# Kernel optimization log

Measured on AMD Instinct MI355X. Metric: run time of the kernel, lower is better.

The kernel has to match this reference:

```python
import jax, jax.numpy as jnp
import numpy as np

EPS = 1e-6

def ln(x):
    m = jnp.mean(x, axis=-1, keepdims=True)
    v = jnp.var(x, axis=-1, keepdims=True)
    return (x - m) * jax.lax.rsqrt(v + EPS)

def modulate(x, shift, scale):
    return x * (1.0 + scale[:, None, :]) + shift[:, None, :]

def setup_inputs() -> dict:
    key = jax.random.key(0)
    ks = jax.random.split(key, 16)
    B, N, H = 2, 384, 256
    D = 128  # n_vector_features * scale_dist_features
    MIN = 2 * H + D  # 640
    FH = 1024  # swiglu_correction_fn(4.0, 256)
    s = 0.02
    inp = {
        "mask": jnp.ones((B, N), jnp.float32),
        "x": jax.random.normal(ks[0], (B, N, H), jnp.float32),
        "t_emb": jax.random.normal(ks[1], (B, H), jnp.float32),
        "dist": jax.random.normal(ks[2], (B, N, N, D), jnp.float32),
        "edge_mask": jnp.ones((B, N, N), jnp.float32),
        "W_ada": jax.random.normal(ks[3], (6 * H, H), jnp.float32) * s,
        "b_ada": jnp.zeros((6 * H,), jnp.float32),
        "W_fe1": jax.random.normal(ks[4], (H, MIN), jnp.float32) * s,
        "b_fe1": jnp.zeros((H,), jnp.float32),
        "W_fe2": jax.random.normal(ks[5], (H, H), jnp.float32) * s,
        "b_fe2": jnp.zeros((H,), jnp.float32),
        "W_qkv": jax.random.normal(ks[6], (3 * H, H), jnp.float32) * s,
        "W_out": jax.random.normal(ks[7], (H, H), jnp.float32) * s,
        "W_ffn1": jax.random.normal(ks[8], (2 * FH, H), jnp.float32) * s,
        "W_ffn2": jax.random.normal(ks[9], (H, FH), jnp.float32) * s,
    }
    return inp

def reference(mask, x, t_emb, dist, edge_mask, W_ada, b_ada, W_fe1, b_fe1,
              W_fe2, b_fe2, W_qkv, W_out, W_ffn1, W_ffn2):
    B, N, H = x.shape
    num_heads = 8
    d_head = H // num_heads
    mN = mask[..., None]  # (B,N,1)

    # adaLN modulation
    ada = jax.nn.silu(t_emb) @ W_ada.T + b_ada  # (B,6H)
    shift_msa, scale_msa, gate_msa, shift_mlp, scale_mlp, gate_mlp = jnp.split(ada, 6, axis=1)

    x_norm = modulate(ln(x * mN), shift_msa, scale_msa)  # (B,N,H)

    # all-pairs message passing: concat(h_i, h_j, dist_ij) -> MLP -> sum_j
    h1 = jnp.broadcast_to(x_norm[:, :, None, :], (B, N, N, H))
    h2 = jnp.broadcast_to(x_norm[:, None, :, :], (B, N, N, H))
    feats = jnp.concatenate([h1, h2, dist], axis=-1) * edge_mask[..., None]
    msgs = jax.nn.silu(feats @ W_fe1.T + b_fe1) @ W_fe2.T + b_fe2  # (B,N,N,H)
    x_msg = jnp.sum(msgs, axis=-2)  # (B,N,H)

    # attention
    qkv = x_msg @ W_qkv.T
    Q, K, V = jnp.split(qkv, 3, axis=-1)
    Q = ln(Q * mN)
    K = ln(K * mN)
    def heads(t):
        return t.reshape(B, N, num_heads, d_head).transpose(0, 2, 1, 3)  # b h s d
    Q, K, V = heads(Q), heads(K), heads(V)
    scores = jnp.einsum("bhqd,bhkd->bhqk", Q, K) / jnp.sqrt(jnp.float32(d_head))
    bias = jnp.where(mask[:, None, None, :] > 0, 0.0, -1e9)
    attn = jax.nn.softmax(scores + bias, axis=-1)
    ao = jnp.einsum("bhqk,bhkd->bhqd", attn, V)
    ao = ao.transpose(0, 2, 1, 3).reshape(B, N, H)
    y = ao @ W_out.T

    x = x + gate_msa[:, None, :] * y

    # SwiGLU FFN
    xm = modulate(ln(x * mN), shift_mlp, scale_mlp)
    h12 = xm @ W_ffn1.T
    h_a, h_b = jnp.split(h12, 2, axis=-1)
    ffn_out = (jax.nn.silu(h_a) * h_b) @ W_ffn2.T
    x = (x + gate_mlp[:, None, :] * ffn_out) * mN
    return x
```

## Files before the change

### kernel.cpp

```cpp
#include <hip/hip_runtime.h>

#define DEVI __device__ __forceinline__

typedef float fv4 __attribute__((ext_vector_type(4)));
typedef __bf16 bf16x8 __attribute__((ext_vector_type(8)));
typedef unsigned short u16x8 __attribute__((ext_vector_type(8)));
typedef unsigned short u16x4 __attribute__((ext_vector_type(4)));

DEVI fv4 ldv4(const float* p) { return *reinterpret_cast<const fv4*>(p); }
DEVI bf16x8 pkbf(fv4 a, fv4 b) {
  bf16x8 r;
  r[0] = (__bf16)a[0]; r[1] = (__bf16)a[1]; r[2] = (__bf16)a[2]; r[3] = (__bf16)a[3];
  r[4] = (__bf16)b[0]; r[5] = (__bf16)b[1]; r[6] = (__bf16)b[2]; r[7] = (__bf16)b[3];
  return r;
}
DEVI u16x8 b2u(bf16x8 v) { return __builtin_bit_cast(u16x8, v); }
DEVI bf16x8 asbf(u16x8 u) { return __builtin_bit_cast(bf16x8, u); }
DEVI unsigned short bfbits(float x) { __bf16 v = (__bf16)x; return __builtin_bit_cast(unsigned short, v); }
DEVI u16x4 pk4(fv4 a) {
  u16x4 u;
  u[0] = bfbits(a[0]); u[1] = bfbits(a[1]); u[2] = bfbits(a[2]); u[3] = bfbits(a[3]);
  return u;
}
DEVI fv4 MFMA16(bf16x8 a, bf16x8 b, fv4 c) {
  return __builtin_amdgcn_mfma_f32_16x16x32_bf16(a, b, c, 0, 0, 0);
}
DEVI float siluf(float x) {
  float e = __builtin_amdgcn_exp2f(x * -1.44269504f);
  return x * __builtin_amdgcn_rcpf(1.f + e);
}
DEVI fv4 glu4(fv4 x, fv4 y) {
  fv4 r;
#pragma unroll
  for (int j = 0; j < 4; ++j) r[j] = siluf(x[j]) * y[j];
  return r;
}
DEVI void lbar() {
  asm volatile("s_waitcnt lgkmcnt(0)" ::: "memory");
  __builtin_amdgcn_s_barrier();
}
DEVI int swz(int row, int k) {
  int unit = k >> 3;
  int phys = (unit & ~7) | ((unit ^ row) & 7);
  return row * 384 + (phys << 3) + (k & 7);
}

__global__ __launch_bounds__(256)
void k_ada(const float* __restrict__ temb, const float* __restrict__ W_ada,
           const float* __restrict__ b_ada, float* __restrict__ ada) {
  __shared__ float sm[256];
  const int b = blockIdx.x / 6;
  const int r = (blockIdx.x % 6) * 256 + threadIdx.x;
  sm[threadIdx.x] = siluf(temb[b * 256 + threadIdx.x]);
  __syncthreads();
  float s = b_ada[r];
  const float* wr = W_ada + (size_t)r * 256;
  for (int k = 0; k < 256; ++k) s += sm[k] * wr[k];
  ada[b * 1536 + r] = s;
}

__global__ __launch_bounds__(256)
void k_xnorm(const float* __restrict__ xin, const float* __restrict__ mask,
             const float* __restrict__ ada, int shift_off, int scale_off,
             float* __restrict__ out) {
  const int row = blockIdx.x;
  const int b = row / 384;
  const int t = threadIdx.x;
  const float m = mask[row];
  const float v = xin[(size_t)row * 256 + t] * m;
  float s = v, ss = v * v;
#pragma unroll
  for (int o = 1; o < 64; o <<= 1) { s += __shfl_xor(s, o); ss += __shfl_xor(ss, o); }
  __shared__ float red[8];
  const int wid = t >> 6;
  if ((t & 63) == 0) { red[wid] = s; red[4 + wid] = ss; }
  __syncthreads();
  s = red[0] + red[1] + red[2] + red[3];
  ss = red[4] + red[5] + red[6] + red[7];
  const float mean = s * (1.f / 256.f);
  const float var = ss * (1.f / 256.f) - mean * mean;
  const float rs = rsqrtf(var + 1e-6f);
  out[(size_t)row * 256 + t] =
      (v - mean) * rs * (1.f + ada[b * 1536 + scale_off + t]) + ada[b * 1536 + shift_off + t];
}

template <int EPI, int AMODE>
__global__ __launch_bounds__(256)
void k_gemm(const float* __restrict__ A, int lda,
            const float* __restrict__ B, int ldb, int koff, int K,
            float* __restrict__ C, int ldc,
            const float* __restrict__ bias, float bscale,
            const float* __restrict__ res,
            const float* __restrict__ ada, int gate_off,
            const float* __restrict__ mask) {
  __shared__ __align__(16) unsigned short As[64 * 64];
  __shared__ __align__(16) unsigned short Bs[64 * 64];
  const int t = threadIdx.x, lane = t & 63, w = t >> 6;
  const int bn0 = blockIdx.x * 64, bm0 = blockIdx.y * 64;
  const int qr = (w >> 1) * 32, qc = (w & 1) * 32;
  const int g = lane >> 4, c = lane & 15;
  const int srow = t >> 2;
  const int so = (t & 3) * 2;
  const int o0 = so ^ (srow & 7), o1 = (so + 1) ^ (srow & 7);
  unsigned short* aw0 = As + srow * 64 + o0 * 8;
  unsigned short* aw1 = As + srow * 64 + o1 * 8;
  unsigned short* bw0 = Bs + srow * 64 + o0 * 8;
  unsigned short* bw1 = Bs + srow * 64 + o1 * 8;
  const float* ag = A + (size_t)(bm0 + srow) * lda + so * 8;
  const float* bg = B + (size_t)(bn0 + srow) * ldb + koff + so * 8;
  const float* a2g = nullptr;
  if constexpr (AMODE == 2) a2g = res + ((size_t)(bm0 + srow) * lda + so * 8);
  fv4 a0 = ldv4(ag), a1 = ldv4(ag + 4), a2 = ldv4(ag + 8), a3 = ldv4(ag + 12);
  fv4 x0, x1, x2, x3;
  if constexpr (AMODE == 1) {
    x0 = ldv4(ag + 1024); x1 = ldv4(ag + 1028); x2 = ldv4(ag + 1032); x3 = ldv4(ag + 1036);
  }
  if constexpr (AMODE == 2) {
    x0 = ldv4(a2g); x1 = ldv4(a2g + 4); x2 = ldv4(a2g + 8); x3 = ldv4(a2g + 12);
  }
  fv4 c0 = ldv4(bg), c1 = ldv4(bg + 4), c2 = ldv4(bg + 8), c3 = ldv4(bg + 12);
  fv4 acc[2][2] = {};
  for (int k0 = 0; k0 < K; k0 += 64) {
    lbar();
    if constexpr (AMODE == 1) {
      *reinterpret_cast<u16x8*>(aw0) = b2u(pkbf(glu4(a0, x0), glu4(a1, x1)));
      *reinterpret_cast<u16x8*>(aw1) = b2u(pkbf(glu4(a2, x2), glu4(a3, x3)));
    } else if constexpr (AMODE == 2) {
      *reinterpret_cast<u16x8*>(aw0) = b2u(pkbf(a0 + x0, a1 + x1));
      *reinterpret_cast<u16x8*>(aw1) = b2u(pkbf(a2 + x2, a3 + x3));
    } else {
      *reinterpret_cast<u16x8*>(aw0) = b2u(pkbf(a0, a1));
      *reinterpret_cast<u16x8*>(aw1) = b2u(pkbf(a2, a3));
    }
    *reinterpret_cast<u16x8*>(bw0) = b2u(pkbf(c0, c1));
    *reinterpret_cast<u16x8*>(bw1) = b2u(pkbf(c2, c3));
    lbar();
    if (k0 + 64 < K) {
      ag += 64; bg += 64;
      a0 = ldv4(ag); a1 = ldv4(ag + 4); a2 = ldv4(ag + 8); a3 = ldv4(ag + 12);
      if constexpr (AMODE == 1) {
        x0 = ldv4(ag + 1024); x1 = ldv4(ag + 1028); x2 = ldv4(ag + 1032); x3 = ldv4(ag + 1036);
      }
      if constexpr (AMODE == 2) {
        a2g += 64;
        x0 = ldv4(a2g); x1 = ldv4(a2g + 4); x2 = ldv4(a2g + 8); x3 = ldv4(a2g + 12);
      }
      c0 = ldv4(bg); c1 = ldv4(bg + 4); c2 = ldv4(bg + 8); c3 = ldv4(bg + 12);
    }
#pragma unroll
    for (int kk = 0; kk < 2; ++kk) {
      bf16x8 af[2], bf[2];
#pragma unroll
      for (int mi = 0; mi < 2; ++mi) {
        int row = qr + mi * 16 + c;
        int oct = (kk * 4 + g) ^ (row & 7);
        af[mi] = asbf(*reinterpret_cast<const u16x8*>(As + row * 64 + oct * 8));
      }
#pragma unroll
      for (int ni = 0; ni < 2; ++ni) {
        int row = qc + ni * 16 + c;
        int oct = (kk * 4 + g) ^ (row & 7);
        bf[ni] = asbf(*reinterpret_cast<const u16x8*>(Bs + row * 64 + oct * 8));
      }
#pragma unroll
      for (int mi = 0; mi < 2; ++mi)
#pragma unroll
        for (int ni = 0; ni < 2; ++ni)
          acc[mi][ni] = MFMA16(af[mi], bf[ni], acc[mi][ni]);
    }
  }
#pragma unroll
  for (int mi = 0; mi < 2; ++mi)
#pragma unroll
    for (int ni = 0; ni < 2; ++ni)
#pragma unroll
      for (int r = 0; r < 4; ++r) {
        int row = bm0 + qr + mi * 16 + g * 4 + r;
        int col = bn0 + qc + ni * 16 + c;
        float v = acc[mi][ni][r];
        if constexpr (EPI == 1) v += bscale * bias[col];
        if constexpr (EPI == 2) v = res[(size_t)row * 256 + col] + ada[(row / 384) * 1536 + gate_off + col] * v;
        if constexpr (EPI == 3) v = (res[(size_t)row * 256 + col] + ada[(row / 384) * 1536 + gate_off + col] * v) * mask[row];
        if constexpr (EPI == 5) C[(((size_t)(row >> 4) * 256 + col) << 4) + (row & 15)] = v;
        else C[(size_t)row * ldc + col] = v;
      }
}

__global__ __launch_bounds__(512)
void k_edge(const float* __restrict__ dist, const float* __restrict__ emask,
            const float* __restrict__ Wfe1, const float* __restrict__ bfe1,
            const float* __restrict__ P, const float* __restrict__ Qc,
            float* __restrict__ S0, float* __restrict__ S1) {
  const int blk = blockIdx.x, jh = blockIdx.y;
  const int b = blk / 384, i = blk - b * 384;
  const int t = threadIdx.x, lane = t & 63, w = t >> 6;
  const int g = lane >> 4, c = lane & 15;
  __shared__ __align__(16) unsigned short Al[2][16 * 128];

  bf16x8 Bf[2][4];
  float Pl[2], bl[2], Ss[2] = {0.f, 0.f};
#pragma unroll
  for (int ht = 0; ht < 2; ++ht) {
    const int h = w * 32 + ht * 16 + c;
    const float* wp = Wfe1 + (size_t)h * 640 + 512 + g * 8;
#pragma unroll
    for (int ks = 0; ks < 4; ++ks)
      Bf[ht][ks] = pkbf(ldv4(wp + ks * 32), ldv4(wp + ks * 32 + 4));
    Pl[ht] = P[(size_t)(b * 384 + i) * 256 + h];
    bl[ht] = bfe1[h];
  }
  const float* dbase = dist + (size_t)(b * 384 + i) * 49152 + (size_t)jh * 24576;
  const float* embase = emask + (size_t)(b * 384 + i) * 384 + jh * 192;
  const int jcb = b * 24 + jh * 12;
  const int h0 = w * 32 + c, h1 = h0 + 16;

  const int srow = t >> 5, kq = t & 31;
  const int sunit = kq >> 1;
  const int sphys = (sunit & 8) | ((sunit ^ (srow & 7)) & 7);
  const int soff = srow * 128 + sphys * 8 + (kq & 1) * 4;

  fv4 rX, rY, qvX0, qvX1, qvY0, qvY1, emX, emY;
  {
    fv4 t0 = ldv4(dbase + t * 4);
    *reinterpret_cast<u16x4*>(&Al[0][soff]) = pk4(t0);
  }
  rX = ldv4(dbase + 2048 + t * 4);
  qvX0 = ldv4(Qc + (((size_t)jcb * 256 + h0) << 4) + g * 4);
  qvX1 = ldv4(Qc + (((size_t)jcb * 256 + h1) << 4) + g * 4);
  emX = ldv4(embase + g * 4);
  lbar();

#pragma unroll 1
  for (int p = 0; p < 6; ++p) {
    {
      const int cl = 2 * p;
      if (cl <= 9) rY = ldv4(dbase + (size_t)(cl + 2) * 2048 + t * 4);
      if (cl <= 10) {
        *reinterpret_cast<u16x4*>(&Al[1][soff]) = pk4(rX);
        const size_t jc = (size_t)(jcb + cl + 1);
        qvY0 = ldv4(Qc + ((jc * 256 + h0) << 4) + g * 4);
        qvY1 = ldv4(Qc + ((jc * 256 + h1) << 4) + g * 4);
        emY = ldv4(embase + (cl + 1) * 16 + g * 4);
      }
      fv4 acc0, acc1;
#pragma unroll
      for (int r = 0; r < 4; ++r) { acc0[r] = Pl[0] + qvX0[r]; acc1[r] = Pl[1] + qvX1[r]; }
#pragma unroll
      for (int ks = 0; ks < 4; ++ks) {
        const int u = ks * 4 + g;
        const int phys = (u & 8) | ((u ^ (c & 7)) & 7);
        bf16x8 af = asbf(*reinterpret_cast<const u16x8*>(&Al[0][c * 128 + phys * 8]));
        acc0 = MFMA16(af, Bf[0][ks], acc0);
        acc1 = MFMA16(af, Bf[1][ks], acc1);
      }
#pragma unroll
      for (int r = 0; r < 4; ++r) {
        Ss[0] += siluf(emX[r] * acc0[r] + bl[0]);
        Ss[1] += siluf(emX[r] * acc1[r] + bl[1]);
      }
      lbar();
    }
    {
      const int cl = 2 * p + 1;
      if (cl <= 9) rX = ldv4(dbase + (size_t)(cl + 2) * 2048 + t * 4);
      if (cl <= 10) {
        *reinterpret_cast<u16x4*>(&Al[0][soff]) = pk4(rY);
        const size_t jc = (size_t)(jcb + cl + 1);
        qvX0 = ldv4(Qc + ((jc * 256 + h0) << 4) + g * 4);
        qvX1 = ldv4(Qc + ((jc * 256 + h1) << 4) + g * 4);
        emX = ldv4(embase + (cl + 1) * 16 + g * 4);
      }
      fv4 acc0, acc1;
#pragma unroll
      for (int r = 0; r < 4; ++r) { acc0[r] = Pl[0] + qvY0[r]; acc1[r] = Pl[1] + qvY1[r]; }
#pragma unroll
      for (int ks = 0; ks < 4; ++ks) {
        const int u = ks * 4 + g;
        const int phys = (u & 8) | ((u ^ (c & 7)) & 7);
        bf16x8 af = asbf(*reinterpret_cast<const u16x8*>(&Al[1][c * 128 + phys * 8]));
        acc0 = MFMA16(af, Bf[0][ks], acc0);
        acc1 = MFMA16(af, Bf[1][ks], acc1);
      }
#pragma unroll
      for (int r = 0; r < 4; ++r) {
        Ss[0] += siluf(emY[r] * acc0[r] + bl[0]);
        Ss[1] += siluf(emY[r] * acc1[r] + bl[1]);
      }
      lbar();
    }
  }
  float* Sp = jh ? S1 : S0;
#pragma unroll
  for (int ht = 0; ht < 2; ++ht) {
    float s = Ss[ht];
    s += __shfl_xor(s, 16);
    s += __shfl_xor(s, 32);
    if (g == 0) Sp[(size_t)(b * 384 + i) * 256 + w * 32 + ht * 16 + c] = s;
  }
}

__global__ __launch_bounds__(256)
void k_lnqk(const float* __restrict__ qkv, const float* __restrict__ mask,
            float* __restrict__ Qn, float* __restrict__ Kn) {
  const int row = blockIdx.x, t = threadIdx.x;
  const float m = mask[row];
  const float q = qkv[(size_t)row * 768 + t] * m;
  const float k = qkv[(size_t)row * 768 + 256 + t] * m;
  float sq = q, sqq = q * q, sk = k, skk = k * k;
#pragma unroll
  for (int o = 1; o < 64; o <<= 1) {
    sq += __shfl_xor(sq, o); sqq += __shfl_xor(sqq, o);
    sk += __shfl_xor(sk, o); skk += __shfl_xor(skk, o);
  }
  __shared__ float red[16];
  const int wid = t >> 6;
  if ((t & 63) == 0) { red[wid] = sq; red[4 + wid] = sqq; red[8 + wid] = sk; red[12 + wid] = skk; }
  __syncthreads();
  sq = red[0] + red[1] + red[2] + red[3];
  sqq = red[4] + red[5] + red[6] + red[7];
  sk = red[8] + red[9] + red[10] + red[11];
  skk = red[12] + red[13] + red[14] + red[15];
  const float mq = sq * (1.f / 256.f), vq = sqq * (1.f / 256.f) - mq * mq;
  const float mk = sk * (1.f / 256.f), vk = skk * (1.f / 256.f) - mk * mk;
  Qn[(size_t)row * 256 + t] = (q - mq) * rsqrtf(vq + 1e-6f);
  Kn[(size_t)row * 256 + t] = (k - mk) * rsqrtf(vk + 1e-6f);
}

__global__ __launch_bounds__(256)
void k_attn(const float* __restrict__ Qn, const float* __restrict__ Kn,
            const float* __restrict__ qkv, const float* __restrict__ mask,
            float* __restrict__ ao) {
  const int bh = blockIdx.y, b = bh >> 3, h = bh & 7;
  const int qg = blockIdx.x;
  const int t = threadIdx.x, lane = t & 63, w = t >> 6;
  const int g = lane >> 4, c = lane & 15;
  __shared__ __align__(16) unsigned short Vt[32 * 384];
  __shared__ __align__(16) unsigned short pl[16 * 384];
  __shared__ float outp[4][16][32];
  __shared__ float redm[4][16], reds[4][16];
  {
    const int d0 = (t & 7) * 4;
    const int kp = t >> 3;
#pragma unroll
    for (int pass = 0; pass < 6; ++pass) {
      int k = pass * 64 + kp * 2;
      fv4 v0 = ldv4(qkv + (size_t)(b * 384 + k) * 768 + 512 + h * 32 + d0);
      fv4 v1 = ldv4(qkv + (size_t)(b * 384 + k + 1) * 768 + 512 + h * 32 + d0);
#pragma unroll
      for (int j = 0; j < 4; ++j) {
        int d = d0 + j;
        unsigned int pr = (unsigned int)bfbits(v0[j]) | ((unsigned int)bfbits(v1[j]) << 16);
        *reinterpret_cast<unsigned int*>(&Vt[swz(d, k)]) = pr;
      }
    }
  }
  bf16x8 qf;
  {
    const float* qp = Qn + (size_t)(b * 384 + qg * 16 + c) * 256 + h * 32 + g * 8;
    qf = pkbf(ldv4(qp), ldv4(qp + 4));
  }
  fv4 sc[6];
#pragma unroll
  for (int kb = 0; kb < 6; ++kb) {
    const float* kp2 = Kn + (size_t)(b * 384 + w * 96 + kb * 16 + c) * 256 + h * 32 + g * 8;
    bf16x8 kf = pkbf(ldv4(kp2), ldv4(kp2 + 4));
    fv4 z = {0.f, 0.f, 0.f, 0.f};
    sc[kb] = MFMA16(qf, kf, z);
  }
  const float rs = 0.1767766952966369f;
  float zz[6][4], mx[4] = {-3e38f, -3e38f, -3e38f, -3e38f};
#pragma unroll
  for (int kb = 0; kb < 6; ++kb) {
    float mb = mask[b * 384 + w * 96 + kb * 16 + c] > 0.f ? 0.f : -1e9f;
#pragma unroll
    for (int r = 0; r < 4; ++r) {
      zz[kb][r] = sc[kb][r] * rs + mb;
      mx[r] = fmaxf(mx[r], zz[kb][r]);
    }
  }
#pragma unroll
  for (int r = 0; r < 4; ++r) {
#pragma unroll
    for (int o = 1; o < 16; o <<= 1) mx[r] = fmaxf(mx[r], __shfl_xor(mx[r], o));
  }
  if (c == 0) {
#pragma unroll
    for (int r = 0; r < 4; ++r) redm[w][g * 4 + r] = mx[r];
  }
  __syncthreads();
  float m4[4], sm[4] = {0.f, 0.f, 0.f, 0.f};
#pragma unroll
  for (int r = 0; r < 4; ++r) {
    int q = g * 4 + r;
    m4[r] = fmaxf(fmaxf(redm[0][q], redm[1][q]), fmaxf(redm[2][q], redm[3][q]));
  }
#pragma unroll
  for (int kb = 0; kb < 6; ++kb) {
    int k = w * 96 + kb * 16 + c;
#pragma unroll
    for (int r = 0; r < 4; ++r) {
      float p = __builtin_amdgcn_exp2f((zz[kb][r] - m4[r]) * 1.44269504f);
      sm[r] += p;
      pl[swz(g * 4 + r, k)] = bfbits(p);
    }
  }
#pragma unroll
  for (int r = 0; r < 4; ++r) {
#pragma unroll
    for (int o = 1; o < 16; o <<= 1) sm[r] += __shfl_xor(sm[r], o);
  }
  if (c == 0) {
#pragma unroll
    for (int r = 0; r < 4; ++r) reds[w][g * 4 + r] = sm[r];
  }
  __syncthreads();
  fv4 oacc[2] = {};
#pragma unroll
  for (int kk = 0; kk < 3; ++kk) {
    int kbase = w * 96 + kk * 32 + g * 8;
    bf16x8 pa = asbf(*reinterpret_cast<const u16x8*>(&pl[swz(c, kbase)]));
#pragma unroll
    for (int db = 0; db < 2; ++db) {
      int d = db * 16 + c;
      bf16x8 vb = asbf(*reinterpret_cast<const u16x8*>(&Vt[swz(d, kbase)]));
      oacc[db] = MFMA16(pa, vb, oacc[db]);
    }
  }
#pragma unroll
  for (int db = 0; db < 2; ++db)
#pragma unroll
    for (int r = 0; r < 4; ++r) outp[w][g * 4 + r][db * 16 + c] = oacc[db][r];
  __syncthreads();
#pragma unroll
  for (int idx = t; idx < 512; idx += 256) {
    int q = idx >> 5, d = idx & 31;
    float v = outp[0][q][d] + outp[1][q][d] + outp[2][q][d] + outp[3][q][d];
    float s = reds[0][q] + reds[1][q] + reds[2][q] + reds[3][q];
    ao[(size_t)(b * 384 + qg * 16 + q) * 256 + h * 32 + d] = v / s;
  }
}

extern "C" void kernel_launch(void* const* d_in, const int* in_sizes, int n_in,
                              void* d_out, int out_size, void* d_ws, size_t ws_size,
                              hipStream_t stream) {
  (void)in_sizes; (void)n_in; (void)out_size; (void)ws_size;
  const float* mask   = (const float*)d_in[0];
  const float* x      = (const float*)d_in[1];
  const float* temb   = (const float*)d_in[2];
  const float* dist   = (const float*)d_in[3];
  const float* emask  = (const float*)d_in[4];
  const float* W_ada  = (const float*)d_in[5];
  const float* b_ada  = (const float*)d_in[6];
  const float* W_fe1  = (const float*)d_in[7];
  const float* b_fe1  = (const float*)d_in[8];
  const float* W_fe2  = (const float*)d_in[9];
  const float* b_fe2  = (const float*)d_in[10];
  const float* W_qkv  = (const float*)d_in[11];
  const float* W_out  = (const float*)d_in[12];
  const float* W_ffn1 = (const float*)d_in[13];
  const float* W_ffn2 = (const float*)d_in[14];
  float* out = (float*)d_out;
  float* ws = (float*)d_ws;

  float* ada   = ws;
  float* xattn = ws + 4096;
  float* xm    = ws + 200704;
  float* xn    = ws + 397312;
  float* P     = ws + 593920;
  float* Qc    = ws + 790528;
  float* S0    = ws + 987136;
  float* xmsg  = ws + 1183744;
  float* qkvb  = ws + 1380352;
  float* Qn    = ws + 1970176;
  float* Kn    = ws + 2166784;
  float* aob   = ws + 2363392;
  float* S1    = ws + 2363392;
  float* h12   = ws + 397312;

  k_ada<<<12, 256, 0, stream>>>(temb, W_ada, b_ada, ada);
  k_xnorm<<<768, 256, 0, stream>>>(x, mask, ada, 0, 256, xn);
  k_gemm<0, 0><<<dim3(4, 12), 256, 0, stream>>>(xn, 256, W_fe1, 640, 0, 256, P, 256,
                                                nullptr, 0.f, nullptr, nullptr, 0, nullptr);
  k_gemm<5, 0><<<dim3(4, 12), 256, 0, stream>>>(xn, 256, W_fe1, 640, 256, 256, Qc, 0,
                                                nullptr, 0.f, nullptr, nullptr, 0, nullptr);
  k_edge<<<dim3(768, 2), 512, 0, stream>>>(dist, emask, W_fe1, b_fe1, P, Qc, S0, S1);
  k_gemm<1, 2><<<dim3(4, 12), 256, 0, stream>>>(S0, 256, W_fe2, 256, 0, 256, xmsg, 256,
                                                b_fe2, 384.f, S1, nullptr, 0, nullptr);
  k_gemm<0, 0><<<dim3(12, 12), 256, 0, stream>>>(xmsg, 256, W_qkv, 256, 0, 256, qkvb, 768,
                                                 nullptr, 0.f, nullptr, nullptr, 0, nullptr);
  k_lnqk<<<768, 256, 0, stream>>>(qkvb, mask, Qn, Kn);
  k_attn<<<dim3(24, 16), 256, 0, stream>>>(Qn, Kn, qkvb, mask, aob);
  k_gemm<2, 0><<<dim3(4, 12), 256, 0, stream>>>(aob, 256, W_out, 256, 0, 256, xattn, 256,
                                                nullptr, 0.f, x, ada, 512, nullptr);
  k_xnorm<<<768, 256, 0, stream>>>(xattn, mask, ada, 768, 1024, xm);
  k_gemm<0, 0><<<dim3(32, 12), 256, 0, stream>>>(xm, 256, W_ffn1, 256, 0, 256, h12, 2048,
                                                 nullptr, 0.f, nullptr, nullptr, 0, nullptr);
  k_gemm<3, 1><<<dim3(4, 12), 256, 0, stream>>>(h12, 2048, W_ffn2, 1024, 0, 1024, out, 256,
                                                nullptr, 0.f, xattn, ada, 1280, mask);
}
```

Before: 149.9 us.

## Process two j-chunks per edge-kernel step and merge the P/Qc GEMMs

The edge kernel now stages 32 rows of dist per iteration instead of 16. That halves the number of barrier-separated steps and issues four MFMAs per k-step sharing each B fragment, with wider 16-byte LDS stores. It also requests 3 blocks per CU through launch bounds. The two GEMMs producing P and Qc are fused into one launch with a split epilogue, saving a kernel launch. In exchange it uses more registers and twice the LDS per block, which could constrain occupancy.

```diff
diff --git a/kernel.cpp b/kernel.cpp
--- a/kernel.cpp
+++ b/kernel.cpp
@@ -17,11 +17,6 @@
 DEVI u16x8 b2u(bf16x8 v) { return __builtin_bit_cast(u16x8, v); }
 DEVI bf16x8 asbf(u16x8 u) { return __builtin_bit_cast(bf16x8, u); }
 DEVI unsigned short bfbits(float x) { __bf16 v = (__bf16)x; return __builtin_bit_cast(unsigned short, v); }
-DEVI u16x4 pk4(fv4 a) {
-  u16x4 u;
-  u[0] = bfbits(a[0]); u[1] = bfbits(a[1]); u[2] = bfbits(a[2]); u[3] = bfbits(a[3]);
-  return u;
-}
 DEVI fv4 MFMA16(bf16x8 a, bf16x8 b, fv4 c) {
   return __builtin_amdgcn_mfma_f32_16x16x32_bf16(a, b, c, 0, 0, 0);
 }
@@ -107,7 +102,12 @@
   unsigned short* bw0 = Bs + srow * 64 + o0 * 8;
   unsigned short* bw1 = Bs + srow * 64 + o1 * 8;
   const float* ag = A + (size_t)(bm0 + srow) * lda + so * 8;
-  const float* bg = B + (size_t)(bn0 + srow) * ldb + koff + so * 8;
+  const int vrow = bn0 + srow;
+  const float* bg;
+  if constexpr (EPI == 7)
+    bg = B + (size_t)(vrow & 255) * ldb + (vrow >> 8) * 256 + so * 8;
+  else
+    bg = B + (size_t)vrow * ldb + koff + so * 8;
   const float* a2g = nullptr;
   if constexpr (AMODE == 2) a2g = res + ((size_t)(bm0 + srow) * lda + so * 8);
   fv4 a0 = ldv4(ag), a1 = ldv4(ag + 4), a2 = ldv4(ag + 8), a3 = ldv4(ag + 12);
@@ -178,15 +178,19 @@
         int row = bm0 + qr + mi * 16 + g * 4 + r;
         int col = bn0 + qc + ni * 16 + c;
         float v = acc[mi][ni][r];
-        if constexpr (EPI == 1) v += bscale * bias[col];
-        if constexpr (EPI == 2) v = res[(size_t)row * 256 + col] + ada[(row / 384) * 1536 + gate_off + col] * v;
-        if constexpr (EPI == 3) v = (res[(size_t)row * 256 + col] + ada[(row / 384) * 1536 + gate_off + col] * v) * mask[row];
-        if constexpr (EPI == 5) C[(((size_t)(row >> 4) * 256 + col) << 4) + (row & 15)] = v;
-        else C[(size_t)row * ldc + col] = v;
-      }
-}
-
-__global__ __launch_bounds__(512)
+        if constexpr (EPI == 7) {
+          if (col < 256) C[(size_t)row * ldc + col] = v;
+          else ((float*)res)[(((size_t)(row >> 4) * 256 + (col - 256)) << 4) + (row & 15)] = v;
+        } else {
+          if constexpr (EPI == 1) v += bscale * bias[col];
+          if constexpr (EPI == 2) v = res[(size_t)row * 256 + col] + ada[(row / 384) * 1536 + gate_off + col] * v;
+          if constexpr (EPI == 3) v = (res[(size_t)row * 256 + col] + ada[(row / 384) * 1536 + gate_off + col] * v) * mask[row];
+          C[(size_t)row * ldc + col] = v;
+        }
+      }
+}
+
+__global__ __launch_bounds__(512, 3)
 void k_edge(const float* __restrict__ dist, const float* __restrict__ emask,
             const float* __restrict__ Wfe1, const float* __restrict__ bfe1,
             const float* __restrict__ P, const float* __restrict__ Qc,
@@ -195,7 +199,7 @@
   const int b = blk / 384, i = blk - b * 384;
   const int t = threadIdx.x, lane = t & 63, w = t >> 6;
   const int g = lane >> 4, c = lane & 15;
-  __shared__ __align__(16) unsigned short Al[2][16 * 128];
+  __shared__ __align__(16) unsigned short Al[2][32 * 128];
 
   bf16x8 Bf[2][4];
   float Pl[2], bl[2], Ss[2] = {0.f, 0.f};
@@ -214,77 +218,110 @@
   const int jcb = b * 24 + jh * 12;
   const int h0 = w * 32 + c, h1 = h0 + 16;
 
-  const int srow = t >> 5, kq = t & 31;
-  const int sunit = kq >> 1;
-  const int sphys = (sunit & 8) | ((sunit ^ (srow & 7)) & 7);
-  const int soff = srow * 128 + sphys * 8 + (kq & 1) * 4;
-
-  fv4 rX, rY, qvX0, qvX1, qvY0, qvY1, emX, emY;
+  const int srow = t >> 4, su = t & 15;
+  const int sphys = (su & 8) | ((su ^ (srow & 7)) & 7);
+  const int soff = srow * 128 + sphys * 8;
+  const float* sg = dbase + srow * 128 + su * 8;
+
+  fv4 rX0, rX1, rY0, rY1;
+  fv4 qvX0, qvX1, qvX2, qvX3, qvY0, qvY1, qvY2, qvY3;
+  fv4 emX0, emX1, emY0, emY1;
+
   {
-    fv4 t0 = ldv4(dbase + t * 4);
-    *reinterpret_cast<u16x4*>(&Al[0][soff]) = pk4(t0);
-  }
-  rX = ldv4(dbase + 2048 + t * 4);
-  qvX0 = ldv4(Qc + (((size_t)jcb * 256 + h0) << 4) + g * 4);
-  qvX1 = ldv4(Qc + (((size_t)jcb * 256 + h1) << 4) + g * 4);
-  emX = ldv4(embase + g * 4);
+    fv4 d0 = ldv4(sg), d1 = ldv4(sg + 4);
+    rX0 = ldv4(sg + 4096); rX1 = ldv4(sg + 4096 + 4);
+    {
+      const size_t jc = (size_t)jcb;
+      qvX0 = ldv4(Qc + ((jc * 256 + h0) << 4) + g * 4);
+      qvX1 = ldv4(Qc + ((jc * 256 + h1) << 4) + g * 4);
+      qvX2 = ldv4(Qc + (((jc + 1) * 256 + h0) << 4) + g * 4);
+      qvX3 = ldv4(Qc + (((jc + 1) * 256 + h1) << 4) + g * 4);
+    }
+    emX0 = ldv4(embase + g * 4);
+    emX1 = ldv4(embase + 16 + g * 4);
+    *reinterpret_cast<u16x8*>(&Al[0][soff]) = b2u(pkbf(d0, d1));
+  }
   lbar();
 
 #pragma unroll 1
-  for (int p = 0; p < 6; ++p) {
+  for (int p = 0; p < 3; ++p) {
     {
       const int cl = 2 * p;
-      if (cl <= 9) rY = ldv4(dbase + (size_t)(cl + 2) * 2048 + t * 4);
-      if (cl <= 10) {
-        *reinterpret_cast<u16x4*>(&Al[1][soff]) = pk4(rX);
-        const size_t jc = (size_t)(jcb + cl + 1);
+      if (cl <= 4) *reinterpret_cast<u16x8*>(&Al[1][soff]) = b2u(pkbf(rX0, rX1));
+      if (cl <= 3) {
+        rY0 = ldv4(sg + (size_t)(cl + 2) * 4096);
+        rY1 = ldv4(sg + (size_t)(cl + 2) * 4096 + 4);
+      }
+      if (cl <= 4) {
+        const size_t jc = (size_t)(jcb + (cl + 1) * 2);
         qvY0 = ldv4(Qc + ((jc * 256 + h0) << 4) + g * 4);
         qvY1 = ldv4(Qc + ((jc * 256 + h1) << 4) + g * 4);
-        emY = ldv4(embase + (cl + 1) * 16 + g * 4);
-      }
-      fv4 acc0, acc1;
-#pragma unroll
-      for (int r = 0; r < 4; ++r) { acc0[r] = Pl[0] + qvX0[r]; acc1[r] = Pl[1] + qvX1[r]; }
+        qvY2 = ldv4(Qc + (((jc + 1) * 256 + h0) << 4) + g * 4);
+        qvY3 = ldv4(Qc + (((jc + 1) * 256 + h1) << 4) + g * 4);
+        emY0 = ldv4(embase + (cl + 1) * 32 + g * 4);
+        emY1 = ldv4(embase + (cl + 1) * 32 + 16 + g * 4);
+      }
+      fv4 a00, a01, a10, a11;
+#pragma unroll
+      for (int r = 0; r < 4; ++r) {
+        a00[r] = Pl[0] + qvX0[r]; a01[r] = Pl[1] + qvX1[r];
+        a10[r] = Pl[0] + qvX2[r]; a11[r] = Pl[1] + qvX3[r];
+      }
 #pragma unroll
       for (int ks = 0; ks < 4; ++ks) {
         const int u = ks * 4 + g;
         const int phys = (u & 8) | ((u ^ (c & 7)) & 7);
-        bf16x8 af = asbf(*reinterpret_cast<const u16x8*>(&Al[0][c * 128 + phys * 8]));
-        acc0 = MFMA16(af, Bf[0][ks], acc0);
-        acc1 = MFMA16(af, Bf[1][ks], acc1);
+        bf16x8 af0 = asbf(*reinterpret_cast<const u16x8*>(&Al[0][c * 128 + phys * 8]));
+        bf16x8 af1 = asbf(*reinterpret_cast<const u16x8*>(&Al[0][(16 + c) * 128 + phys * 8]));
+        a00 = MFMA16(af0, Bf[0][ks], a00); a01 = MFMA16(af0, Bf[1][ks], a01);
+        a10 = MFMA16(af1, Bf[0][ks], a10); a11 = MFMA16(af1, Bf[1][ks], a11);
       }
 #pragma unroll
       for (int r = 0; r < 4; ++r) {
-        Ss[0] += siluf(emX[r] * acc0[r] + bl[0]);
-        Ss[1] += siluf(emX[r] * acc1[r] + bl[1]);
+        Ss[0] += siluf(emX0[r] * a00[r] + bl[0]);
+        Ss[1] += siluf(emX0[r] * a01[r] + bl[1]);
+        Ss[0] += siluf(emX1[r] * a10[r] + bl[0]);
+        Ss[1] += siluf(emX1[r] * a11[r] + bl[1]);
       }
       lbar();
     }
     {
       const int cl = 2 * p + 1;
-      if (cl <= 9) rX = ldv4(dbase + (size_t)(cl + 2) * 2048 + t * 4);
-      if (cl <= 10) {
-        *reinterpret_cast<u16x4*>(&Al[0][soff]) = pk4(rY);
-        const size_t jc = (size_t)(jcb + cl + 1);
+      if (cl <= 4) *reinterpret_cast<u16x8*>(&Al[0][soff]) = b2u(pkbf(rY0, rY1));
+      if (cl <= 3) {
+        rX0 = ldv4(sg + (size_t)(cl + 2) * 4096);
+        rX1 = ldv4(sg + (size_t)(cl + 2) * 4096 + 4);
+      }
+      if (cl <= 4) {
+        const size_t jc = (size_t)(jcb + (cl + 1) * 2);
         qvX0 = ldv4(Qc + ((jc * 256 + h0) << 4) + g * 4);
         qvX1 = ldv4(Qc + ((jc * 256 + h1) << 4) + g * 4);
-        emX = ldv4(embase + (cl + 1) * 16 + g * 4);
-      }
-      fv4 acc0, acc1;
-#pragma unroll
-      for (int r = 0; r < 4; ++r) { acc0[r] = Pl[0] + qvY0[r]; acc1[r] = Pl[1] + qvY1[r]; }
+        qvX2 = ldv4(Qc + (((jc + 1) * 256 + h0) << 4) + g * 4);
+        qvX3 = ldv4(Qc + (((jc + 1) * 256 + h1) << 4) + g * 4);
+        emX0 = ldv4(embase + (cl + 1) * 32 + g * 4);
+        emX1 = ldv4(embase + (cl + 1) * 32 + 16 + g * 4);
+      }
+      fv4 a00, a01, a10, a11;
+#pragma unroll
+      for (int r = 0; r < 4; ++r) {
+        a00[r] = Pl[0] + qvY0[r]; a01[r] = Pl[1] + qvY1[r];
+        a10[r] = Pl[0] + qvY2[r]; a11[r] = Pl[1] + qvY3[r];
+      }
 #pragma unroll
       for (int ks = 0; ks < 4; ++ks) {
         const int u = ks * 4 + g;
         const int phys = (u & 8) | ((u ^ (c & 7)) & 7);
-        bf16x8 af = asbf(*reinterpret_cast<const u16x8*>(&Al[1][c * 128 + phys * 8]));
-        acc0 = MFMA16(af, Bf[0][ks], acc0);
-        acc1 = MFMA16(af, Bf[1][ks], acc1);
+        bf16x8 af0 = asbf(*reinterpret_cast<const u16x8*>(&Al[1][c * 128 + phys * 8]));
+        bf16x8 af1 = asbf(*reinterpret_cast<const u16x8*>(&Al[1][(16 + c) * 128 + phys * 8]));
+        a00 = MFMA16(af0, Bf[0][ks], a00); a01 = MFMA16(af0, Bf[1][ks], a01);
+        a10 = MFMA16(af1, Bf[0][ks], a10); a11 = MFMA16(af1, Bf[1][ks], a11);
       }
 #pragma unroll
       for (int r = 0; r < 4; ++r) {
-        Ss[0] += siluf(emY[r] * acc0[r] + bl[0]);
-        Ss[1] += siluf(emY[r] * acc1[r] + bl[1]);
+        Ss[0] += siluf(emY0[r] * a00[r] + bl[0]);
+        Ss[1] += siluf(emY0[r] * a01[r] + bl[1]);
+        Ss[0] += siluf(emY1[r] * a10[r] + bl[0]);
+        Ss[1] += siluf(emY1[r] * a11[r] + bl[1]);
       }
       lbar();
     }
@@ -479,10 +516,8 @@
 
   k_ada<<<12, 256, 0, stream>>>(temb, W_ada, b_ada, ada);
   k_xnorm<<<768, 256, 0, stream>>>(x, mask, ada, 0, 256, xn);
-  k_gemm<0, 0><<<dim3(4, 12), 256, 0, stream>>>(xn, 256, W_fe1, 640, 0, 256, P, 256,
-                                                nullptr, 0.f, nullptr, nullptr, 0, nullptr);
-  k_gemm<5, 0><<<dim3(4, 12), 256, 0, stream>>>(xn, 256, W_fe1, 640, 256, 256, Qc, 0,
-                                                nullptr, 0.f, nullptr, nullptr, 0, nullptr);
+  k_gemm<7, 0><<<dim3(8, 12), 256, 0, stream>>>(xn, 256, W_fe1, 640, 0, 256, P, 256,
+                                                nullptr, 0.f, Qc, nullptr, 0, nullptr);
   k_edge<<<dim3(768, 2), 512, 0, stream>>>(dist, emask, W_fe1, b_fe1, P, Qc, S0, S1);
   k_gemm<1, 2><<<dim3(4, 12), 256, 0, stream>>>(S0, 256, W_fe2, 256, 0, 256, xmsg, 256,
                                                 b_fe2, 384.f, S1, nullptr, 0, nullptr);
```

Result: slower. 163.2 us (+8.9%).
